# Kernel tuning notes

Hardware: AMD Instinct MI355X
Metric: run time of the kernel (lower is better)

The kernel has to match this reference:

```python
import jax, jax.numpy as jnp
import numpy as np

NUM_EXPERTS = 8
DIM = 1024
HIDDEN = 2048
N_TOKENS = 8192  # rows of x, includes padding beyond sum(num_tokens_per_expert)


def setup_inputs() -> dict:
    key = jax.random.key(0)
    k_x, k_w1, k_w2, k_w3 = jax.random.split(key, 4)
    x = jax.random.normal(k_x, (N_TOKENS, DIM), dtype=jnp.float32)
    # trunc_normal(std=0.02)-like init; w2 is zeros in torch init but we use
    w1 = jax.random.normal(k_w1, (NUM_EXPERTS, HIDDEN, DIM), dtype=jnp.float32) * 0.02
    w2 = jax.random.normal(k_w2, (NUM_EXPERTS, DIM, HIDDEN), dtype=jnp.float32) * 0.02
    w3 = jax.random.normal(k_w3, (NUM_EXPERTS, HIDDEN, DIM), dtype=jnp.float32) * 0.02
    # routed token counts per expert; sum <= N_TOKENS, remainder is padding
    num_tokens_per_expert = jnp.array([995, 1000, 980, 1010, 970, 1020, 990, 1005], dtype=jnp.int64)
    return {"x": x, "num_tokens_per_expert": num_tokens_per_expert,
            "w1": w1, "w2": w2, "w3": w3}


def reference(x, num_tokens_per_expert, w1, w2, w3):
    # Mirrors torch _run_experts_for_loop with act='silu'. The torch code calls
    # .tolist() on the counts (shapes are data-dependent), so we likewise treat
    # the per-expert counts as static host values.
    counts = np.asarray(num_tokens_per_expert).astype(np.int64)
    offsets = np.concatenate([np.zeros(1, np.int64), np.cumsum(counts)])
    total = int(offsets[-1])
    num_experts = w1.shape[0]
    out_splits = []
    for e in range(num_experts):
        xe = x[int(offsets[e]):int(offsets[e + 1])]            # [n_e, dim]
        gate = jax.nn.silu(xe @ w1[e].T)                       # [n_e, hidden]
        h = gate * (xe @ w3[e].T)                              # SwiGLU
        out_splits.append(h @ w2[e].T)                         # [n_e, dim]
    out = jnp.concatenate(out_splits, axis=0)
    num_padding = x.shape[0] - total
    if num_padding > 0:
        out = jnp.concatenate([out, jnp.zeros((num_padding, out.shape[-1]), out.dtype)], axis=0)
    return out
```

## Files before the change

kernel.cpp:

```cpp
#include <hip/hip_runtime.h>

#define NEXP 8
#define DIM  1024
#define HID  2048
#define NTOK 8192

#define BM 128
#define BN 128
#define BK 32
#define LDK 40

typedef short s16x8 __attribute__((ext_vector_type(8)));
typedef float f32x4 __attribute__((ext_vector_type(4)));
typedef unsigned short u16;

__device__ __forceinline__ u16 f2bf(float f) {
  unsigned int u = __builtin_bit_cast(unsigned int, f);
  u += 0x7FFFu + ((u >> 16) & 1u);
  return (u16)(u >> 16);
}

__device__ __forceinline__ void gload16(const u16* g, u16* l) {
  __builtin_amdgcn_global_load_lds((const __attribute__((address_space(1))) void*)g,
                                   (__attribute__((address_space(3))) void*)l, 16, 0, 0);
}

__device__ __forceinline__ bool find_tile(const int* __restrict__ cnts, int rt,
                                          int& e_out, int& row0, int& cnt_out, long long& off_out) {
  long long off = 0; int cum = 0;
  #pragma unroll
  for (int e = 0; e < NEXP; ++e) {
    int c = cnts[e];
    int nt = (c + BM - 1) / BM;
    if (rt < cum + nt) { e_out = e; row0 = (rt - cum) * BM; cnt_out = c; off_out = off; return true; }
    cum += nt; off += c;
  }
  return false;
}

__device__ __forceinline__ void cvt8(const float* __restrict__ s, u16* __restrict__ d, int j) {
  const float4* p = (const float4*)s + 2 * (size_t)j;
  const float4 a = p[0], b = p[1];
  s16x8 v;
  v[0] = (short)f2bf(a.x); v[1] = (short)f2bf(a.y); v[2] = (short)f2bf(a.z); v[3] = (short)f2bf(a.w);
  v[4] = (short)f2bf(b.x); v[5] = (short)f2bf(b.y); v[6] = (short)f2bf(b.z); v[7] = (short)f2bf(b.w);
  *((s16x8*)d + (size_t)j) = v;
}

__global__ __launch_bounds__(256) void cvt_multi(
    const float* __restrict__ s0, u16* __restrict__ d0, int n0,
    const float* __restrict__ s1, u16* __restrict__ d1, int n1,
    const float* __restrict__ s2, u16* __restrict__ d2, int n2,
    const float* __restrict__ s3, u16* __restrict__ d3, int n3) {
  const int b0 = n0, b1 = b0 + n1, b2 = b1 + n2, b3 = b2 + n3;
  for (int i = blockIdx.x * blockDim.x + threadIdx.x; i < b3; i += gridDim.x * blockDim.x) {
    if      (i < b0) cvt8(s0, d0, i);
    else if (i < b1) cvt8(s1, d1, i - b0);
    else if (i < b2) cvt8(s2, d2, i - b1);
    else             cvt8(s3, d3, i - b2);
  }
}

#define XSTR 68
__global__ __launch_bounds__(512, 4) void gemm1_bf16(
    const u16* __restrict__ xb, const int* __restrict__ cnts,
    const u16* __restrict__ w1b, const u16* __restrict__ w3b,
    u16* __restrict__ hbuf)
{
  int e, row0, cnt; long long off;
  if (!find_tile(cnts, blockIdx.y, e, row0, cnt, off)) return;
  const int ct = blockIdx.x;

  __shared__ float smem_f[4 * 64 * XSTR];
  u16* stage = (u16*)smem_f;

  const int t    = threadIdx.x;
  const int lane = t & 63;
  const int wid  = t >> 6;
  const int mat  = wid >> 2;
  const int sw   = wid & 3;
  const int wr = sw >> 1, wc = sw & 1;
  const int lr = lane & 15;
  const int lk = (lane >> 4) * 8;

  const u16* xrow = xb + (size_t)(off + row0) * DIM;
  const u16* w1t  = w1b + ((size_t)e * HID + (size_t)ct * BN) * DIM;
  const u16* w3t  = w3b + ((size_t)e * HID + (size_t)ct * BN) * DIM;

  f32x4 acc[4][4];
  const f32x4 zf = {0.f, 0.f, 0.f, 0.f};
  #pragma unroll
  for (int i = 0; i < 4; ++i)
    #pragma unroll
    for (int j = 0; j < 4; ++j) acc[i][j] = zf;

  const int sidx = wid * 512 + lane * 8;
  const int srow = sidx >> 5;
  const int scol = sidx & 31;

  auto STAGE = [&](int k0, int b) {
    u16* base = stage + b * (3 * 4096);
    const size_t go = (size_t)srow * DIM + k0 + scol;
    gload16(&xrow[go], base        + wid * 512);
    gload16(&w1t [go], base + 4096 + wid * 512);
    gload16(&w3t [go], base + 8192 + wid * 512);
  };

  STAGE(0, 0);
  __syncthreads();
  int cur = 0;
  const int NT = DIM / BK;
  for (int kt = 0; kt < NT; ++kt) {
    if (kt + 1 < NT) STAGE((kt + 1) * BK, cur ^ 1);

    const u16* Asb = stage + cur * (3 * 4096);
    const u16* Bsb = Asb + 4096 + mat * 4096;
    s16x8 af[4], bf[4];
    #pragma unroll
    for (int fm = 0; fm < 4; ++fm)
      af[fm] = *(const s16x8*)&Asb[(wr * 64 + fm * 16 + lr) * BK + lk];
    #pragma unroll
    for (int fn = 0; fn < 4; ++fn)
      bf[fn] = *(const s16x8*)&Bsb[(wc * 64 + fn * 16 + lr) * BK + lk];
    #pragma unroll
    for (int fm = 0; fm < 4; ++fm)
      #pragma unroll
      for (int fn = 0; fn < 4; ++fn)
        acc[fm][fn] = __builtin_amdgcn_mfma_f32_16x16x32_bf16(af[fm], bf[fn], acc[fm][fn], 0, 0, 0);

    __syncthreads();
    cur ^= 1;
  }

  if (mat) {
    float* up = smem_f + sw * (64 * XSTR);
    #pragma unroll
    for (int fm = 0; fm < 4; ++fm)
      #pragma unroll
      for (int fn = 0; fn < 4; ++fn)
        #pragma unroll
        for (int j = 0; j < 4; ++j)
          up[(fm * 16 + ((lane >> 4) << 2) + j) * XSTR + fn * 16 + lr] = acc[fm][fn][j];
  }
  __syncthreads();
  if (!mat) {
    const float* up = smem_f + sw * (64 * XSTR);
    #pragma unroll
    for (int fm = 0; fm < 4; ++fm)
      #pragma unroll
      for (int fn = 0; fn < 4; ++fn) {
        const int col = ct * BN + wc * 64 + fn * 16 + lr;
        #pragma unroll
        for (int j = 0; j < 4; ++j) {
          const int r = wr * 64 + fm * 16 + ((lane >> 4) << 2) + j;
          if (row0 + r < cnt) {
            const float gv = acc[fm][fn][j];
            const float uv = up[(fm * 16 + ((lane >> 4) << 2) + j) * XSTR + fn * 16 + lr];
            const float hv = (gv / (1.f + __expf(-gv))) * uv;
            hbuf[(size_t)(off + row0 + r) * HID + col] = f2bf(hv);
          }
        }
      }
  }
}

__global__ __launch_bounds__(256) void gemm2_bf16(
    const u16* __restrict__ hbuf, const int* __restrict__ cnts,
    const u16* __restrict__ w2b, float* __restrict__ out)
{
  int e, row0, cnt; long long off;
  if (!find_tile(cnts, blockIdx.y, e, row0, cnt, off)) return;
  const int ct = blockIdx.x;

  __shared__ u16 stage[2 * 2 * BM * BK];

  const int t    = threadIdx.x;
  const int lane = t & 63;
  const int wid  = t >> 6;
  const int wr = wid >> 1, wc = wid & 1;
  const int lr = lane & 15;
  const int lk = (lane >> 4) * 8;

  const u16* arow = hbuf + (size_t)(off + row0) * HID;
  const u16* w2t  = w2b + ((size_t)e * DIM + (size_t)ct * BN) * HID;

  f32x4 acc[4][4];
  const f32x4 zf = {0.f, 0.f, 0.f, 0.f};
  #pragma unroll
  for (int i = 0; i < 4; ++i)
    #pragma unroll
    for (int j = 0; j < 4; ++j) acc[i][j] = zf;

  auto STAGE = [&](int k0, int b) {
    u16* base = stage + b * (2 * 4096);
    #pragma unroll
    for (int c = 0; c < 2; ++c) {
      const int chunk = wid * 2 + c;
      const int idx   = chunk * 512 + lane * 8;
      const int r  = idx >> 5;
      const int cc = idx & 31;
      const size_t go = (size_t)r * HID + k0 + cc;
      gload16(&arow[go], base        + chunk * 512);
      gload16(&w2t [go], base + 4096 + chunk * 512);
    }
  };

  STAGE(0, 0);
  __syncthreads();
  int cur = 0;
  const int NT = HID / BK;
  for (int kt = 0; kt < NT; ++kt) {
    if (kt + 1 < NT) STAGE((kt + 1) * BK, cur ^ 1);

    const u16* Asb = stage + cur * (2 * 4096);
    const u16* Bsb = Asb + 4096;
    s16x8 af[4], bf[4];
    #pragma unroll
    for (int fm = 0; fm < 4; ++fm)
      af[fm] = *(const s16x8*)&Asb[(wr * 64 + fm * 16 + lr) * BK + lk];
    #pragma unroll
    for (int fn = 0; fn < 4; ++fn)
      bf[fn] = *(const s16x8*)&Bsb[(wc * 64 + fn * 16 + lr) * BK + lk];
    #pragma unroll
    for (int fm = 0; fm < 4; ++fm)
      #pragma unroll
      for (int fn = 0; fn < 4; ++fn)
        acc[fm][fn] = __builtin_amdgcn_mfma_f32_16x16x32_bf16(af[fm], bf[fn], acc[fm][fn], 0, 0, 0);

    __syncthreads();
    cur ^= 1;
  }

  #pragma unroll
  for (int fm = 0; fm < 4; ++fm)
    #pragma unroll
    for (int fn = 0; fn < 4; ++fn) {
      const int col = ct * BN + wc * 64 + fn * 16 + lr;
      #pragma unroll
      for (int j = 0; j < 4; ++j) {
        const int r = wr * 64 + fm * 16 + ((lane >> 4) << 2) + j;
        if (row0 + r < cnt)
          out[(size_t)(off + row0 + r) * DIM + col] = acc[fm][fn][j];
      }
    }
}

__global__ __launch_bounds__(256) void gemm1_kernel(
    const float* __restrict__ x, const int* __restrict__ cnts,
    const float* __restrict__ w1, const float* __restrict__ w3,
    u16* __restrict__ hbuf)
{
  int e, row0, cnt; long long off;
  if (!find_tile(cnts, blockIdx.y, e, row0, cnt, off)) return;
  const int ct = blockIdx.x;

  __shared__ u16 As [BM * LDK];
  __shared__ u16 B1s[BN * LDK];
  __shared__ u16 B3s[BN * LDK];

  const int t    = threadIdx.x;
  const int srow = t >> 3;
  const int skq  = (t & 7) * 4;
  const int lane = t & 63;
  const int wid  = t >> 6;
  const int wr = wid >> 1, wc = wid & 1;
  const int lr = lane & 15;
  const int lk = (lane >> 4) * 8;

  const float* w1e = w1 + (size_t)e * HID * DIM;
  const float* w3e = w3 + (size_t)e * HID * DIM;

  f32x4 accg[4][4], accu[4][4];
  const f32x4 zf = {0.f, 0.f, 0.f, 0.f};
  #pragma unroll
  for (int i = 0; i < 4; ++i)
    #pragma unroll
    for (int j = 0; j < 4; ++j) { accg[i][j] = zf; accu[i][j] = zf; }

  for (int k0 = 0; k0 < DIM; k0 += BK) {
    __syncthreads();
    #pragma unroll
    for (int s = 0; s < 4; ++s) {
      const int r = s * 32 + srow;
      float4 va = make_float4(0.f, 0.f, 0.f, 0.f);
      const int gm = row0 + r;
      if (gm < cnt) va = *(const float4*)&x[(size_t)(off + gm) * DIM + k0 + skq];
      ushort4 ua; ua.x = f2bf(va.x); ua.y = f2bf(va.y); ua.z = f2bf(va.z); ua.w = f2bf(va.w);
      *(ushort4*)&As[r * LDK + skq] = ua;
      const size_t gb = (size_t)(ct * BN + r) * DIM + k0 + skq;
      const float4 v1 = *(const float4*)&w1e[gb];
      const float4 v3 = *(const float4*)&w3e[gb];
      ushort4 u1; u1.x = f2bf(v1.x); u1.y = f2bf(v1.y); u1.z = f2bf(v1.z); u1.w = f2bf(v1.w);
      ushort4 u3; u3.x = f2bf(v3.x); u3.y = f2bf(v3.y); u3.z = f2bf(v3.z); u3.w = f2bf(v3.w);
      *(ushort4*)&B1s[r * LDK + skq] = u1;
      *(ushort4*)&B3s[r * LDK + skq] = u3;
    }
    __syncthreads();

    s16x8 af[4], b1f[4], b3f[4];
    #pragma unroll
    for (int fm = 0; fm < 4; ++fm)
      af[fm] = *(const s16x8*)&As[(wr * 64 + fm * 16 + lr) * LDK + lk];
    #pragma unroll
    for (int fn = 0; fn < 4; ++fn) {
      b1f[fn] = *(const s16x8*)&B1s[(wc * 64 + fn * 16 + lr) * LDK + lk];
      b3f[fn] = *(const s16x8*)&B3s[(wc * 64 + fn * 16 + lr) * LDK + lk];
    }
    #pragma unroll
    for (int fm = 0; fm < 4; ++fm)
      #pragma unroll
      for (int fn = 0; fn < 4; ++fn) {
        accg[fm][fn] = __builtin_amdgcn_mfma_f32_16x16x32_bf16(af[fm], b1f[fn], accg[fm][fn], 0, 0, 0);
        accu[fm][fn] = __builtin_amdgcn_mfma_f32_16x16x32_bf16(af[fm], b3f[fn], accu[fm][fn], 0, 0, 0);
      }
  }

  #pragma unroll
  for (int fm = 0; fm < 4; ++fm)
    #pragma unroll
    for (int fn = 0; fn < 4; ++fn) {
      const f32x4 g = accg[fm][fn], u = accu[fm][fn];
      const int col = ct * BN + wc * 64 + fn * 16 + lr;
      #pragma unroll
      for (int j = 0; j < 4; ++j) {
        const int r = wr * 64 + fm * 16 + ((lane >> 4) << 2) + j;
        if (row0 + r < cnt) {
          const float gv = g[j];
          const float hv = (gv / (1.f + __expf(-gv))) * u[j];
          hbuf[(size_t)(off + row0 + r) * HID + col] = f2bf(hv);
        }
      }
    }
}

__global__ __launch_bounds__(256) void gemm2_kernel(
    const u16* __restrict__ hbuf, const int* __restrict__ cnts,
    const float* __restrict__ w2, float* __restrict__ out)
{
  int e, row0, cnt; long long off;
  if (!find_tile(cnts, blockIdx.y, e, row0, cnt, off)) return;
  const int ct = blockIdx.x;

  __shared__ u16 As[BM * LDK];
  __shared__ u16 Bs[BN * LDK];

  const int t    = threadIdx.x;
  const int srow = t >> 3;
  const int skq  = (t & 7) * 4;
  const int lane = t & 63;
  const int wid  = t >> 6;
  const int wr = wid >> 1, wc = wid & 1;
  const int lr = lane & 15;
  const int lk = (lane >> 4) * 8;

  const float* w2e = w2 + (size_t)e * DIM * HID;

  f32x4 acc[4][4];
  const f32x4 zf = {0.f, 0.f, 0.f, 0.f};
  #pragma unroll
  for (int i = 0; i < 4; ++i)
    #pragma unroll
    for (int j = 0; j < 4; ++j) acc[i][j] = zf;

  for (int k0 = 0; k0 < HID; k0 += BK) {
    __syncthreads();
    #pragma unroll
    for (int s = 0; s < 4; ++s) {
      const int r = s * 32 + srow;
      ushort4 ua = make_ushort4(0, 0, 0, 0);
      const int gm = row0 + r;
      if (gm < cnt) ua = *(const ushort4*)&hbuf[(size_t)(off + gm) * HID + k0 + skq];
      *(ushort4*)&As[r * LDK + skq] = ua;
      const float4 v2 = *(const float4*)&w2e[(size_t)(ct * BN + r) * HID + k0 + skq];
      ushort4 u2; u2.x = f2bf(v2.x); u2.y = f2bf(v2.y); u2.z = f2bf(v2.z); u2.w = f2bf(v2.w);
      *(ushort4*)&Bs[r * LDK + skq] = u2;
    }
    __syncthreads();

    s16x8 af[4], bf[4];
    #pragma unroll
    for (int fm = 0; fm < 4; ++fm)
      af[fm] = *(const s16x8*)&As[(wr * 64 + fm * 16 + lr) * LDK + lk];
    #pragma unroll
    for (int fn = 0; fn < 4; ++fn)
      bf[fn] = *(const s16x8*)&Bs[(wc * 64 + fn * 16 + lr) * LDK + lk];
    #pragma unroll
    for (int fm = 0; fm < 4; ++fm)
      #pragma unroll
      for (int fn = 0; fn < 4; ++fn)
        acc[fm][fn] = __builtin_amdgcn_mfma_f32_16x16x32_bf16(af[fm], bf[fn], acc[fm][fn], 0, 0, 0);
  }

  #pragma unroll
  for (int fm = 0; fm < 4; ++fm)
    #pragma unroll
    for (int fn = 0; fn < 4; ++fn) {
      const int col = ct * BN + wc * 64 + fn * 16 + lr;
      #pragma unroll
      for (int j = 0; j < 4; ++j) {
        const int r = wr * 64 + fm * 16 + ((lane >> 4) << 2) + j;
        if (row0 + r < cnt)
          out[(size_t)(off + row0 + r) * DIM + col] = acc[fm][fn][j];
      }
    }
}

__global__ void zero_pad_kernel(const int* __restrict__ cnts, float* __restrict__ out)
{
  int total = 0;
  #pragma unroll
  for (int e = 0; e < NEXP; ++e) total += cnts[e];
  const int row = blockIdx.x;
  if (row < total) return;
  float4* p = (float4*)(out + (size_t)row * DIM);
  p[threadIdx.x] = make_float4(0.f, 0.f, 0.f, 0.f);
}

extern "C" void kernel_launch(void* const* d_in, const int* in_sizes, int n_in,
                              void* d_out, int out_size, void* d_ws, size_t ws_size,
                              hipStream_t stream) {
  const float* x    = (const float*)d_in[0];
  const int*   cnts = (const int*)d_in[1];
  const float* w1   = (const float*)d_in[2];
  const float* w2   = (const float*)d_in[3];
  const float* w3   = (const float*)d_in[4];
  float*       out  = (float*)d_out;

  const size_t HBUF_E = (size_t)NTOK * HID;
  const size_t XB_E   = (size_t)NTOK * DIM;
  const size_t W_E    = (size_t)NEXP * HID * DIM;
  const size_t need_min  = (HBUF_E + XB_E + 2 * W_E) * sizeof(u16);
  const size_t need_full = (HBUF_E + XB_E + 3 * W_E) * sizeof(u16);

  u16* hbuf = (u16*)d_ws;
  dim3 blk(256);
  const int XB8 = (int)(XB_E / 8), W8 = (int)(W_E / 8);

  if (ws_size >= need_full) {
    u16* xb = hbuf + HBUF_E;
    u16* wA = xb + XB_E;
    u16* wB = wA + W_E;
    u16* wC = wB + W_E;
    cvt_multi<<<dim3(2048), blk, 0, stream>>>(x, xb, XB8, w1, wA, W8, w3, wB, W8, w2, wC, W8);
    gemm1_bf16<<<dim3(HID / BN, 72), dim3(512), 0, stream>>>(xb, cnts, wA, wB, hbuf);
    gemm2_bf16<<<dim3(DIM / BN, 72), blk, 0, stream>>>(hbuf, cnts, wC, out);
  } else if (ws_size >= need_min) {
    u16* xb = hbuf + HBUF_E;
    u16* wA = xb + XB_E;
    u16* wB = wA + W_E;
    cvt_multi<<<dim3(2048), blk, 0, stream>>>(x, xb, XB8, w1, wA, W8, w3, wB, W8, (const float*)nullptr, (u16*)nullptr, 0);
    gemm1_bf16<<<dim3(HID / BN, 72), dim3(512), 0, stream>>>(xb, cnts, wA, wB, hbuf);
    cvt_multi<<<dim3(2048), blk, 0, stream>>>(w2, wA, W8, (const float*)nullptr, (u16*)nullptr, 0,
                                              (const float*)nullptr, (u16*)nullptr, 0,
                                              (const float*)nullptr, (u16*)nullptr, 0);
    gemm2_bf16<<<dim3(DIM / BN, 72), blk, 0, stream>>>(hbuf, cnts, wA, out);
  } else {
    gemm1_kernel<<<dim3(HID / BN, 72), blk, 0, stream>>>(x, cnts, w1, w3, hbuf);
    gemm2_kernel<<<dim3(DIM / BN, 72), blk, 0, stream>>>(hbuf, cnts, w2, out);
  }
  zero_pad_kernel<<<dim3(NTOK), dim3(256), 0, stream>>>(cnts, out);
}
```

Baseline: 205.4 us.

## Triple-buffer GEMM K-loop with vmcnt waits and widen conversion per thread

Both bf16 GEMM kernels move from double buffering with two __syncthreads per iteration to a three-stage LDS ring. Loads are issued two tiles ahead, and each iteration uses a single s_waitcnt vmcnt plus s_barrier, so global-to-LDS traffic can overlap more MFMA work. The fp32-to-bf16 conversion kernel now handles 32 elements per thread instead of 8 to raise memory-level parallelism, and gemm2 gets a launch-bounds occupancy hint. The extra buffer increases LDS use, which may lower occupancy, and the hand-counted vmcnt values must match the number of loads issued per stage.

```diff
diff --git a/kernel.cpp b/kernel.cpp
--- a/kernel.cpp
+++ b/kernel.cpp
@@ -38,13 +38,21 @@
   return false;
 }
 
-__device__ __forceinline__ void cvt8(const float* __restrict__ s, u16* __restrict__ d, int j) {
-  const float4* p = (const float4*)s + 2 * (size_t)j;
-  const float4 a = p[0], b = p[1];
-  s16x8 v;
-  v[0] = (short)f2bf(a.x); v[1] = (short)f2bf(a.y); v[2] = (short)f2bf(a.z); v[3] = (short)f2bf(a.w);
-  v[4] = (short)f2bf(b.x); v[5] = (short)f2bf(b.y); v[6] = (short)f2bf(b.z); v[7] = (short)f2bf(b.w);
-  *((s16x8*)d + (size_t)j) = v;
+__device__ __forceinline__ void cvt32(const float* __restrict__ s, u16* __restrict__ d, int j) {
+  const float4* p = (const float4*)s + 8 * (size_t)j;
+  float4 a[8];
+  #pragma unroll
+  for (int q = 0; q < 8; ++q) a[q] = p[q];
+  s16x8* dst = (s16x8*)d + 4 * (size_t)j;
+  #pragma unroll
+  for (int q = 0; q < 4; ++q) {
+    s16x8 v;
+    v[0] = (short)f2bf(a[2*q].x);   v[1] = (short)f2bf(a[2*q].y);
+    v[2] = (short)f2bf(a[2*q].z);   v[3] = (short)f2bf(a[2*q].w);
+    v[4] = (short)f2bf(a[2*q+1].x); v[5] = (short)f2bf(a[2*q+1].y);
+    v[6] = (short)f2bf(a[2*q+1].z); v[7] = (short)f2bf(a[2*q+1].w);
+    dst[q] = v;
+  }
 }
 
 __global__ __launch_bounds__(256) void cvt_multi(
@@ -54,10 +62,10 @@
     const float* __restrict__ s3, u16* __restrict__ d3, int n3) {
   const int b0 = n0, b1 = b0 + n1, b2 = b1 + n2, b3 = b2 + n3;
   for (int i = blockIdx.x * blockDim.x + threadIdx.x; i < b3; i += gridDim.x * blockDim.x) {
-    if      (i < b0) cvt8(s0, d0, i);
-    else if (i < b1) cvt8(s1, d1, i - b0);
-    else if (i < b2) cvt8(s2, d2, i - b1);
-    else             cvt8(s3, d3, i - b2);
+    if      (i < b0) cvt32(s0, d0, i);
+    else if (i < b1) cvt32(s1, d1, i - b0);
+    else if (i < b2) cvt32(s2, d2, i - b1);
+    else             cvt32(s3, d3, i - b2);
   }
 }
 
@@ -71,8 +79,9 @@
   if (!find_tile(cnts, blockIdx.y, e, row0, cnt, off)) return;
   const int ct = blockIdx.x;
 
-  __shared__ float smem_f[4 * 64 * XSTR];
-  u16* stage = (u16*)smem_f;
+  __shared__ __align__(16) u16 smem[3 * 3 * 4096];
+  u16* stage = smem;
+  float* smem_f = (float*)smem;
 
   const int t    = threadIdx.x;
   const int lane = t & 63;
@@ -105,15 +114,8 @@
     gload16(&w1t [go], base + 4096 + wid * 512);
     gload16(&w3t [go], base + 8192 + wid * 512);
   };
-
-  STAGE(0, 0);
-  __syncthreads();
-  int cur = 0;
-  const int NT = DIM / BK;
-  for (int kt = 0; kt < NT; ++kt) {
-    if (kt + 1 < NT) STAGE((kt + 1) * BK, cur ^ 1);
-
-    const u16* Asb = stage + cur * (3 * 4096);
+  auto COMPUTE = [&](int b) {
+    const u16* Asb = stage + b * (3 * 4096);
     const u16* Bsb = Asb + 4096 + mat * 4096;
     s16x8 af[4], bf[4];
     #pragma unroll
@@ -127,11 +129,21 @@
       #pragma unroll
       for (int fn = 0; fn < 4; ++fn)
         acc[fm][fn] = __builtin_amdgcn_mfma_f32_16x16x32_bf16(af[fm], bf[fn], acc[fm][fn], 0, 0, 0);
-
-    __syncthreads();
-    cur ^= 1;
-  }
-
+  };
+
+  const int NT = DIM / BK;
+  STAGE(0, 0);
+  STAGE(BK, 1);
+  for (int kt = 0; kt < NT; ++kt) {
+    if (kt == NT - 1) { asm volatile("s_waitcnt vmcnt(0)" ::: "memory"); }
+    else              { asm volatile("s_waitcnt vmcnt(3)" ::: "memory"); }
+    __builtin_amdgcn_s_barrier();
+    asm volatile("" ::: "memory");
+    if (kt + 2 < NT) STAGE((kt + 2) * BK, (kt + 2) % 3);
+    COMPUTE(kt % 3);
+  }
+
+  __syncthreads();
   if (mat) {
     float* up = smem_f + sw * (64 * XSTR);
     #pragma unroll
@@ -164,7 +176,7 @@
   }
 }
 
-__global__ __launch_bounds__(256) void gemm2_bf16(
+__global__ __launch_bounds__(256, 4) void gemm2_bf16(
     const u16* __restrict__ hbuf, const int* __restrict__ cnts,
     const u16* __restrict__ w2b, float* __restrict__ out)
 {
@@ -172,7 +184,7 @@
   if (!find_tile(cnts, blockIdx.y, e, row0, cnt, off)) return;
   const int ct = blockIdx.x;
 
-  __shared__ u16 stage[2 * 2 * BM * BK];
+  __shared__ __align__(16) u16 stage[3 * 2 * 4096];
 
   const int t    = threadIdx.x;
   const int lane = t & 63;
@@ -204,15 +216,8 @@
       gload16(&w2t [go], base + 4096 + chunk * 512);
     }
   };
-
-  STAGE(0, 0);
-  __syncthreads();
-  int cur = 0;
-  const int NT = HID / BK;
-  for (int kt = 0; kt < NT; ++kt) {
-    if (kt + 1 < NT) STAGE((kt + 1) * BK, cur ^ 1);
-
-    const u16* Asb = stage + cur * (2 * 4096);
+  auto COMPUTE = [&](int b) {
+    const u16* Asb = stage + b * (2 * 4096);
     const u16* Bsb = Asb + 4096;
     s16x8 af[4], bf[4];
     #pragma unroll
@@ -226,9 +231,18 @@
       #pragma unroll
       for (int fn = 0; fn < 4; ++fn)
         acc[fm][fn] = __builtin_amdgcn_mfma_f32_16x16x32_bf16(af[fm], bf[fn], acc[fm][fn], 0, 0, 0);
-
-    __syncthreads();
-    cur ^= 1;
+  };
+
+  const int NT = HID / BK;
+  STAGE(0, 0);
+  STAGE(BK, 1);
+  for (int kt = 0; kt < NT; ++kt) {
+    if (kt == NT - 1) { asm volatile("s_waitcnt vmcnt(0)" ::: "memory"); }
+    else              { asm volatile("s_waitcnt vmcnt(4)" ::: "memory"); }
+    __builtin_amdgcn_s_barrier();
+    asm volatile("" ::: "memory");
+    if (kt + 2 < NT) STAGE((kt + 2) * BK, (kt + 2) % 3);
+    COMPUTE(kt % 3);
   }
 
   #pragma unroll
@@ -434,23 +448,23 @@
 
   u16* hbuf = (u16*)d_ws;
   dim3 blk(256);
-  const int XB8 = (int)(XB_E / 8), W8 = (int)(W_E / 8);
+  const int XB32 = (int)(XB_E / 32), W32 = (int)(W_E / 32);
 
   if (ws_size >= need_full) {
     u16* xb = hbuf + HBUF_E;
     u16* wA = xb + XB_E;
     u16* wB = wA + W_E;
     u16* wC = wB + W_E;
-    cvt_multi<<<dim3(2048), blk, 0, stream>>>(x, xb, XB8, w1, wA, W8, w3, wB, W8, w2, wC, W8);
+    cvt_multi<<<dim3(2048), blk, 0, stream>>>(x, xb, XB32, w1, wA, W32, w3, wB, W32, w2, wC, W32);
     gemm1_bf16<<<dim3(HID / BN, 72), dim3(512), 0, stream>>>(xb, cnts, wA, wB, hbuf);
     gemm2_bf16<<<dim3(DIM / BN, 72), blk, 0, stream>>>(hbuf, cnts, wC, out);
   } else if (ws_size >= need_min) {
     u16* xb = hbuf + HBUF_E;
     u16* wA = xb + XB_E;
     u16* wB = wA + W_E;
-    cvt_multi<<<dim3(2048), blk, 0, stream>>>(x, xb, XB8, w1, wA, W8, w3, wB, W8, (const float*)nullptr, (u16*)nullptr, 0);
+    cvt_multi<<<dim3(2048), blk, 0, stream>>>(x, xb, XB32, w1, wA, W32, w3, wB, W32, (const float*)nullptr, (u16*)nullptr, 0);
     gemm1_bf16<<<dim3(HID / BN, 72), dim3(512), 0, stream>>>(xb, cnts, wA, wB, hbuf);
-    cvt_multi<<<dim3(2048), blk, 0, stream>>>(w2, wA, W8, (const float*)nullptr, (u16*)nullptr, 0,
+    cvt_multi<<<dim3(2048), blk, 0, stream>>>(w2, wA, W32, (const float*)nullptr, (u16*)nullptr, 0,
                                               (const float*)nullptr, (u16*)nullptr, 0,
                                               (const float*)nullptr, (u16*)nullptr, 0);
     gemm2_bf16<<<dim3(DIM / BN, 72), blk, 0, stream>>>(hbuf, cnts, wA, out);
```

Result: slower. 213.1 us (+3.7%).
